# Kernel optimization log

Measured on AMD Instinct MI355X. Metric: run time of the kernel, lower is better.

Reference implementation:

```python
import jax, jax.numpy as jnp
import numpy as np

N, F = 8192, 1024


def _lin_params(key, out_f, in_f):
    kw, kb = jax.random.split(key)
    w = jax.random.normal(kw, (out_f, in_f), dtype=jnp.float32) * 0.02
    b = jax.random.normal(kb, (out_f,), dtype=jnp.float32) * 0.02
    return w, b


def setup_inputs() -> dict:
    key = jax.random.key(0)
    ks = jax.random.split(key, 11)
    X = jax.random.normal(ks[0], (N, F), dtype=jnp.float32)
    A = jax.random.uniform(ks[1], (N, N), dtype=jnp.float32)
    W1_w, W1_b = _lin_params(ks[2], 512, F)
    t1_w, t1_b = _lin_params(ks[3], 1, 512)
    r1_w, r1_b = _lin_params(ks[4], 1, 512)
    W2_w, W2_b = _lin_params(ks[5], 256, 512)
    t2_w, t2_b = _lin_params(ks[6], 1, 256)
    r2_w, r2_b = _lin_params(ks[7], 1, 256)
    W3_w, W3_b = _lin_params(ks[8], 64, 256)
    t3_w, t3_b = _lin_params(ks[9], 1, 64)
    r3_w, r3_b = _lin_params(ks[10], 1, 64)
    return dict(X=X, A=A,
                W1_w=W1_w, W1_b=W1_b, t1_w=t1_w, t1_b=t1_b, r1_w=r1_w, r1_b=r1_b,
                W2_w=W2_w, W2_b=W2_b, t2_w=t2_w, t2_b=t2_b, r2_w=r2_w, r2_b=r2_b,
                W3_w=W3_w, W3_b=W3_b, t3_w=t3_w, t3_b=t3_b, r3_w=r3_w, r3_b=r3_b)


def _gat_layer(H, A, W_w, W_b, t_w, t_b, r_w, r_b):
    Z = jax.nn.relu(H @ W_w.T + W_b)                     # [N, out]
    t = (Z @ t_w.T + t_b)[:, 0]                          # [N] = vkt(Z)
    r = (Z @ r_w.T + r_b)[:, 0]                          # [N] = vkr(Z)
    # M_s = A * vkt(Z).T  -> M_s[i,j] = A[i,j] * t[j]
    # M_r = (A * vkr(Z).T).T -> M_r[i,j] = A[j,i] * r[i]
    M = A * t[None, :] + A.T * r[:, None]
    att = jax.nn.softmax(jax.nn.sigmoid(M), axis=1)      # torch default dim=1 for 2D
    return att @ Z


def reference(X, A,
              W1_w, W1_b, t1_w, t1_b, r1_w, r1_b,
              W2_w, W2_b, t2_w, t2_b, r2_w, r2_b,
              W3_w, W3_b, t3_w, t3_b, r3_w, r3_b):
    H1 = _gat_layer(X, A, W1_w, W1_b, t1_w, t1_b, r1_w, r1_b)
    H2 = _gat_layer(H1, A, W2_w, W2_b, t2_w, t2_b, r2_w, r2_b)
    H3 = _gat_layer(H2, A, W3_w, W3_b, t3_w, t3_b, r3_w, r3_b)
    return H3
```

## Files before the change

kernel.cpp:

```cpp
#include <hip/hip_runtime.h>
#include <math.h>

#define NN 8192

typedef __attribute__((ext_vector_type(8))) short short8;
typedef __attribute__((ext_vector_type(4))) float f32x4;

__device__ __forceinline__ float bf2f(unsigned short u) {
    unsigned int x = ((unsigned int)u) << 16;
    return __builtin_bit_cast(float, x);
}
__device__ __forceinline__ unsigned int cvt_pk_bf16(float lo, float hi) {
    unsigned int r;
    asm("v_cvt_pk_bf16_f32 %0, %1, %2" : "=v"(r) : "v"(lo), "v"(hi));
    return r;
}
__device__ __forceinline__ float fast_sigexp(float x) {
    float s = __builtin_amdgcn_rcpf(1.0f + __expf(-x));
    return __expf(s);
}
__device__ __forceinline__ void gload16(const void* g, void* l) {
    __builtin_amdgcn_global_load_lds(
        (const __attribute__((address_space(1))) unsigned int*)g,
        (__attribute__((address_space(3))) unsigned int*)l, 16, 0, 0);
}

__global__ __launch_bounds__(256) void cvt_bf16(
    const float* __restrict__ src, unsigned short* __restrict__ dst)
{
    size_t idx = ((size_t)blockIdx.x * 256 + threadIdx.x) * 8;
    float4 a = *(const float4*)(src + idx);
    float4 b = *(const float4*)(src + idx + 4);
    uint4 o = { cvt_pk_bf16(a.x, a.y), cvt_pk_bf16(a.z, a.w),
                cvt_pk_bf16(b.x, b.y), cvt_pk_bf16(b.z, b.w) };
    *(uint4*)(dst + idx) = o;
}

template<typename AT> struct ARow;
template<> struct ARow<unsigned short> {
    struct Raw { uint4 a, b; };
    static __device__ __forceinline__ Raw ld(const unsigned short* p) {
        Raw r; r.a = ((const uint4*)p)[0]; r.b = ((const uint4*)p)[1]; return r;
    }
    static __device__ __forceinline__ void cvt(const Raw& r, float* d) {
        unsigned int wd[8] = {r.a.x, r.a.y, r.a.z, r.a.w, r.b.x, r.b.y, r.b.z, r.b.w};
        #pragma unroll
        for (int k = 0; k < 8; ++k) {
            d[2*k]   = __builtin_bit_cast(float, wd[k] << 16);
            d[2*k+1] = __builtin_bit_cast(float, wd[k] & 0xFFFF0000u);
        }
    }
};
template<> struct ARow<float> {
    struct Raw { float4 v[4]; };
    static __device__ __forceinline__ Raw ld(const float* p) {
        Raw r;
        r.v[0] = ((const float4*)p)[0]; r.v[1] = ((const float4*)p)[1];
        r.v[2] = ((const float4*)p)[2]; r.v[3] = ((const float4*)p)[3];
        return r;
    }
    static __device__ __forceinline__ void cvt(const Raw& r, float* d) {
        #pragma unroll
        for (int q = 0; q < 4; ++q) {
            d[4*q+0] = r.v[q].x; d[4*q+1] = r.v[q].y;
            d[4*q+2] = r.v[q].z; d[4*q+3] = r.v[q].w;
        }
    }
};
struct AcStageF32 {
    static __device__ __forceinline__ void st(const ARow<float>::Raw& rw, unsigned short* dst) {
        float v[16];
        ARow<float>::cvt(rw, v);
        unsigned int d[8];
        #pragma unroll
        for (int k = 0; k < 8; ++k) d[k] = cvt_pk_bf16(v[2*k], v[2*k+1]);
        uint4 s0 = {d[0], d[1], d[2], d[3]};
        uint4 s1 = {d[4], d[5], d[6], d[7]};
        ((uint4*)dst)[0] = s0;
        ((uint4*)dst)[1] = s1;
    }
};

__global__ __launch_bounds__(256) void proj_mfma(
    const unsigned short* __restrict__ Hbf,
    const unsigned short* __restrict__ Wbf,
    const float* __restrict__ bias,
    unsigned short* __restrict__ Zt,
    int K, int O)
{
    constexpr int MT = 4, NT = 2;
    __shared__ unsigned short smem[12288];
    const int tid = threadIdx.x;
    const int w = tid >> 6;
    const int lane = tid & 63;
    const int quad = lane >> 4;
    const int m16 = lane & 15;
    const int i0 = blockIdx.y * 128;
    const int o0 = blockIdx.x * 64;
    const int wm = w & 1;
    const int wn = w >> 1;

    const char* gpa[2]; unsigned int loa[2];
    #pragma unroll
    for (int n = 0; n < 2; ++n) {
        int o16 = n * 256 + w * 64 + lane;
        int row = o16 >> 2, ch = o16 & 3;
        int sc = ch ^ ((row >> 1) & 3);
        gpa[n] = (const char*)(Hbf + (size_t)(i0 + row) * K) + sc * 16;
        loa[n] = n * 4096 + w * 1024 + lane * 16;
    }
    const char* gpb; unsigned int lob_;
    {
        int o16 = w * 64 + lane;
        int row = o16 >> 2, ch = o16 & 3;
        int sc = ch ^ ((row >> 1) & 3);
        gpb = (const char*)(Wbf + (size_t)(o0 + row) * K) + sc * 16;
        lob_ = 8192 + w * 1024 + lane * 16;
    }
    int aoff[MT], boff[NT];
    #pragma unroll
    for (int mt = 0; mt < MT; ++mt) {
        int row = wm * 64 + mt * 16 + m16;
        int sc = quad ^ ((row >> 1) & 3);
        aoff[mt] = row * 32 + sc * 8;
    }
    #pragma unroll
    for (int nt = 0; nt < NT; ++nt) {
        int row = wn * 32 + nt * 16 + m16;
        int sc = quad ^ ((row >> 1) & 3);
        boff[nt] = 4096 + row * 32 + sc * 8;
    }
    f32x4 acc[MT][NT];
    #pragma unroll
    for (int mt = 0; mt < MT; ++mt)
        #pragma unroll
        for (int nt = 0; nt < NT; ++nt)
            acc[mt][nt] = (f32x4){0.f, 0.f, 0.f, 0.f};

    gload16(gpa[0], (char*)smem + loa[0]);
    gload16(gpa[1], (char*)smem + loa[1]);
    gload16(gpb,    (char*)smem + lob_);
    __syncthreads();

    const int nk = K >> 5;
    for (int kk = 0; kk < nk; ++kk) {
        const int s = kk & 1;
        if (kk + 1 < nk) {
            char* dst = (char*)smem + (s ^ 1) * 12288;
            gload16(gpa[0] + (size_t)(kk + 1) * 64, dst + loa[0]);
            gload16(gpa[1] + (size_t)(kk + 1) * 64, dst + loa[1]);
            gload16(gpb    + (size_t)(kk + 1) * 64, dst + lob_);
        }
        const unsigned short* buf = smem + s * 6144;
        short8 af[MT], bf_[NT];
        #pragma unroll
        for (int mt = 0; mt < MT; ++mt) af[mt] = *(const short8*)(buf + aoff[mt]);
        #pragma unroll
        for (int nt = 0; nt < NT; ++nt) bf_[nt] = *(const short8*)(buf + boff[nt]);
        #pragma unroll
        for (int mt = 0; mt < MT; ++mt)
            #pragma unroll
            for (int nt = 0; nt < NT; ++nt)
                acc[mt][nt] = __builtin_amdgcn_mfma_f32_16x16x32_bf16(
                    af[mt], bf_[nt], acc[mt][nt], 0, 0, 0);
        __syncthreads();
    }
    #pragma unroll
    for (int nt = 0; nt < NT; ++nt) {
        int ol = wn * 32 + nt * 16 + m16;
        float bv = bias[o0 + ol];
        #pragma unroll
        for (int mt = 0; mt < MT; ++mt) {
            int il = wm * 64 + mt * 16 + quad * 4;
            float f0 = fmaxf(acc[mt][nt][0] + bv, 0.f);
            float f1 = fmaxf(acc[mt][nt][1] + bv, 0.f);
            float f2 = fmaxf(acc[mt][nt][2] + bv, 0.f);
            float f3 = fmaxf(acc[mt][nt][3] + bv, 0.f);
            uint2 pk = { cvt_pk_bf16(f0, f1), cvt_pk_bf16(f2, f3) };
            *(uint2*)&smem[ol * 136 + il] = pk;
        }
    }
    __syncthreads();
    #pragma unroll
    for (int c = 0; c < 4; ++c) {
        int cc = c * 256 + tid;
        int ol = cc >> 4;
        int ic = (cc & 15) << 3;
        *(uint4*)(Zt + (size_t)(o0 + ol) * NN + i0 + ic) = *(const uint4*)&smem[ol * 136 + ic];
    }
}

__global__ __launch_bounds__(256) void tr_zt(
    const unsigned short* __restrict__ Zt,
    const float* __restrict__ tw, const float* __restrict__ tb,
    const float* __restrict__ rw, const float* __restrict__ rb,
    float* __restrict__ t, float* __restrict__ r)
{
    const int i  = blockIdx.x * 256 + threadIdx.x;
    const int c0 = blockIdx.y * 64;
    float at = 0.f, ar = 0.f;
    for (int c = c0; c < c0 + 64; ++c) {
        float z = bf2f(Zt[(size_t)c * NN + i]);
        at = fmaf(z, tw[c], at);
        ar = fmaf(z, rw[c], ar);
    }
    if (blockIdx.y == 0) { at += tb[0]; ar += rb[0]; }
    atomicAdd(t + i, at);
    atomicAdd(r + i, ar);
}

template<int BN, typename AT>
__global__ __launch_bounds__(256) void attn_fused(
    const AT* __restrict__ A,
    const unsigned short* __restrict__ Zt,
    const float* __restrict__ t, const float* __restrict__ r,
    float* __restrict__ Hacc, float* __restrict__ denom,
    int O, int kcount)
{
    constexpr bool BFA = (sizeof(AT) == 2);
    constexpr int BM = 128, BK = 32;
    constexpr int MT = 4;
    constexpr int NT = BN / 32;
    constexpr int NB = (BN * BK * 2) / 4096;
    constexpr int BNK = BN * BK;
    __shared__ unsigned short As[BM * BK];
    __shared__ unsigned short Bs[2][BNK];
    __shared__ unsigned short Ac[2][BK * BM];
    const int tid  = threadIdx.x;
    const int w    = tid >> 6;
    const int lane = tid & 63;
    const int quad = lane >> 4;
    const int m16  = lane & 15;
    const int i0 = blockIdx.y * BM;
    const int c0 = blockIdx.x * BN;
    const int wm = w & 1;
    const int wn = w >> 1;
    const int jbase = blockIdx.z * kcount * BK;

    const int ci = tid >> 1;
    const int jh = tid & 1;
    const float ri = r[i0 + ci];
    const int si = (ci >> 1) & 3;
    unsigned short* asw0 = As + ci * 32 + (((jh * 2)    ) ^ si) * 8;
    unsigned short* asw1 = As + ci * 32 + (((jh * 2) + 1) ^ si) * 8;
    const int acrd = jh * 16 * BM + (ci ^ (jh << 5));

    const char* gpb[NB]; unsigned int lob[NB];
    #pragma unroll
    for (int n = 0; n < NB; ++n) {
        int o16 = n * 256 + w * 64 + lane;
        int row = o16 >> 2, ch = o16 & 3;
        int sc = ch ^ ((row >> 1) & 3);
        gpb[n] = (const char*)Zt + ((size_t)(c0 + row) * NN + jbase) * 2 + sc * 16;
        lob[n] = n * 4096 + w * 1024 + lane * 16;
    }
    const char* gpac[2] = {nullptr, nullptr};
    unsigned int loac[2] = {0, 0};
    const float* astage = nullptr;
    int acw_off = 0;
    if constexpr (BFA) {
        #pragma unroll
        for (int n = 0; n < 2; ++n) {
            int o16 = n * 256 + tid;
            int row = o16 >> 4;
            int c16 = (o16 & 15) ^ ((row >> 4) << 2);
            gpac[n] = (const char*)(A + (size_t)(jbase + row) * NN + i0 + c16 * 8);
            loac[n] = (unsigned int)(o16 * 16);
        }
    } else {
        const int sj = tid >> 3;
        const int sm = tid & 7;
        astage = (const float*)A + (size_t)(jbase + sj) * NN + i0 + sm * 16;
        acw_off = sj * BM + (((sm * 2) ^ ((sj >> 4) << 2)) * 8);
    }

    int aoff[MT], boff[NT];
    #pragma unroll
    for (int mt = 0; mt < MT; ++mt) {
        int row = wm * 64 + mt * 16 + m16;
        int sc = quad ^ ((row >> 1) & 3);
        aoff[mt] = row * 32 + sc * 8;
    }
    #pragma unroll
    for (int nt = 0; nt < NT; ++nt) {
        int row = wn * (BN / 2) + nt * 16 + m16;
        int sc = quad ^ ((row >> 1) & 3);
        boff[nt] = row * 32 + sc * 8;
    }

    f32x4 acc[MT][NT];
    #pragma unroll
    for (int mt = 0; mt < MT; ++mt)
        #pragma unroll
        for (int nt = 0; nt < NT; ++nt)
            acc[mt][nt] = (f32x4){0.f, 0.f, 0.f, 0.f};

    const AT* arow = A + (size_t)(i0 + ci) * NN + jbase + jh * 16;
    const float* tptr = t + jbase + jh * 16;

    #pragma unroll
    for (int n = 0; n < NB; ++n)
        gload16(gpb[n], (char*)(Bs[0]) + lob[n]);
    if constexpr (BFA) {
        gload16(gpac[0], (char*)(Ac[0]) + loac[0]);
        gload16(gpac[1], (char*)(Ac[0]) + loac[1]);
    } else {
        ARow<float>::Raw a0 = ARow<float>::ld(astage);
        AcStageF32::st(a0, &Ac[0][0] + acw_off);
    }
    typename ARow<AT>::Raw avr = ARow<AT>::ld(arow);
    float4 tvr0 = ((const float4*)tptr)[0];
    float4 tvr1 = ((const float4*)tptr)[1];
    float4 tvr2 = ((const float4*)tptr)[2];
    float4 tvr3 = ((const float4*)tptr)[3];
    __syncthreads();

    ARow<float>::Raw acr;
    float rsum = 0.f;
    for (int kk = 0; kk < kcount; ++kk) {
        const int b = kk & 1;
        if (kk + 1 < kcount) {
            #pragma unroll
            for (int n = 0; n < NB; ++n)
                gload16(gpb[n] + (size_t)(kk + 1) * 64, (char*)(Bs[b ^ 1]) + lob[n]);
            if constexpr (BFA) {
                gload16(gpac[0] + (size_t)(kk + 1) * (BK * NN * 2), (char*)(Ac[b ^ 1]) + loac[0]);
                gload16(gpac[1] + (size_t)(kk + 1) * (BK * NN * 2), (char*)(Ac[b ^ 1]) + loac[1]);
            } else {
                acr = ARow<float>::ld(astage + (size_t)(kk + 1) * BK * NN);
            }
        }
        float av[16];
        ARow<AT>::cvt(avr, av);
        float tf[16] = {tvr0.x, tvr0.y, tvr0.z, tvr0.w,
                        tvr1.x, tvr1.y, tvr1.z, tvr1.w,
                        tvr2.x, tvr2.y, tvr2.z, tvr2.w,
                        tvr3.x, tvr3.y, tvr3.z, tvr3.w};
        const unsigned short* acb = &Ac[b][0] + acrd;
        unsigned int wd[8];
        #pragma unroll
        for (int q = 0; q < 8; ++q) {
            float j0 = bf2f(acb[(2 * q) * BM]);
            float j1 = bf2f(acb[(2 * q + 1) * BM]);
            float x0 = fmaf(av[2 * q],     tf[2 * q],     j0 * ri);
            float x1 = fmaf(av[2 * q + 1], tf[2 * q + 1], j1 * ri);
            float p0 = fast_sigexp(x0);
            float p1 = fast_sigexp(x1);
            rsum += p0; rsum += p1;
            wd[q] = cvt_pk_bf16(p0, p1);
        }
        {
            uint4 s0 = {wd[0], wd[1], wd[2], wd[3]};
            uint4 s1 = {wd[4], wd[5], wd[6], wd[7]};
            *(uint4*)asw0 = s0;
            *(uint4*)asw1 = s1;
        }
        __syncthreads();
        if (kk + 1 < kcount) {
            avr = ARow<AT>::ld(arow + (size_t)(kk + 1) * BK);
            const float* tp = tptr + (kk + 1) * BK;
            tvr0 = ((const float4*)tp)[0];
            tvr1 = ((const float4*)tp)[1];
            tvr2 = ((const float4*)tp)[2];
            tvr3 = ((const float4*)tp)[3];
            if constexpr (!BFA)
                AcStageF32::st(acr, &Ac[b ^ 1][0] + acw_off);
        }
        {
            const unsigned short* bsb = Bs[b];
            short8 af[MT], bf_[NT];
            #pragma unroll
            for (int mt = 0; mt < MT; ++mt) af[mt] = *(const short8*)(As + aoff[mt]);
            #pragma unroll
            for (int nt = 0; nt < NT; ++nt) bf_[nt] = *(const short8*)(bsb + boff[nt]);
            #pragma unroll
            for (int mt = 0; mt < MT; ++mt)
                #pragma unroll
                for (int nt = 0; nt < NT; ++nt)
                    acc[mt][nt] = __builtin_amdgcn_mfma_f32_16x16x32_bf16(
                        af[mt], bf_[nt], acc[mt][nt], 0, 0, 0);
        }
        __syncthreads();
    }

    rsum += __shfl_xor(rsum, 1);
    if (jh == 0 && blockIdx.x == 0)
        atomicAdd(denom + i0 + ci, rsum);

    const int colb = c0 + wn * (BN / 2) + m16;
    #pragma unroll
    for (int mt = 0; mt < MT; ++mt) {
        int rowb = i0 + wm * 64 + mt * 16 + quad * 4;
        #pragma unroll
        for (int rg = 0; rg < 4; ++rg) {
            float* orow = Hacc + (size_t)(rowb + rg) * O + colb;
            #pragma unroll
            for (int nt = 0; nt < NT; ++nt)
                atomicAdd(orow + nt * 16, acc[mt][nt][rg]);
        }
    }
}

__global__ __launch_bounds__(256) void norm_cvt(
    const float* __restrict__ Hacc, const float* __restrict__ denom,
    float* __restrict__ outf, unsigned short* __restrict__ outb, int O)
{
    const int gid = blockIdx.x * 256 + threadIdx.x;
    const int n4 = O >> 2;
    const int i = gid / n4;
    const int c = (gid % n4) << 2;
    float inv = __builtin_amdgcn_rcpf(denom[i]);
    float4 v = *(const float4*)(Hacc + (size_t)i * O + c);
    v.x *= inv; v.y *= inv; v.z *= inv; v.w *= inv;
    if (outf) {
        *(float4*)(outf + (size_t)i * O + c) = v;
    } else {
        uint2 o = { cvt_pk_bf16(v.x, v.y), cvt_pk_bf16(v.z, v.w) };
        *(uint2*)(outb + (size_t)i * O + c) = o;
    }
}

extern "C" void kernel_launch(void* const* d_in, const int* in_sizes, int n_in,
                              void* d_out, int out_size, void* d_ws, size_t ws_size,
                              hipStream_t stream)
{
    (void)in_sizes; (void)n_in; (void)out_size;
    const float* X = (const float*)d_in[0];
    const float* A = (const float*)d_in[1];
    const float* Wws[3] = {(const float*)d_in[2],  (const float*)d_in[8],  (const float*)d_in[14]};
    const float* Wbs[3] = {(const float*)d_in[3],  (const float*)d_in[9],  (const float*)d_in[15]};
    const float* tws[3] = {(const float*)d_in[4],  (const float*)d_in[10], (const float*)d_in[16]};
    const float* tbs[3] = {(const float*)d_in[5],  (const float*)d_in[11], (const float*)d_in[17]};
    const float* rws[3] = {(const float*)d_in[6],  (const float*)d_in[12], (const float*)d_in[18]};
    const float* rbs[3] = {(const float*)d_in[7],  (const float*)d_in[13], (const float*)d_in[19]};
    const int Ks[3] = {1024, 512, 256};
    const int Os[3] = {512, 256, 64};
    const int Zs[3] = {8, 16, 16};
    float* out = (float*)d_out;
    char* ws = (char*)d_ws;
    const size_t MB = (size_t)1 << 20;

    unsigned short* HbfX = (unsigned short*)(ws);
    unsigned short* Hbf2 = (unsigned short*)(ws + 16 * MB);
    unsigned short* Zt   = (unsigned short*)(ws + 24 * MB);
    float*          Hacc = (float*)(ws + 32 * MB);
    unsigned short* Wbf  = (unsigned short*)(ws + 48 * MB);
    float* tv = (float*)(ws + 50 * MB);
    float* rv = tv + NN;
    float* dv = rv + NN;
    unsigned short* Abf = (unsigned short*)(ws + 51 * MB);
    const bool useAbf = (ws_size >= 180 * MB);

    unsigned short* WbfL[3] = {Wbf, Wbf + 512 * 1024, Wbf + 512 * 1024 + 256 * 512};

    cvt_bf16<<<(NN * 1024) / 2048, 256, 0, stream>>>(X, HbfX);
    for (int L = 0; L < 3; ++L)
        cvt_bf16<<<(Os[L] * Ks[L]) / 2048, 256, 0, stream>>>(Wws[L], WbfL[L]);
    if (useAbf)
        cvt_bf16<<<(int)(((size_t)NN * NN) / 2048), 256, 0, stream>>>(A, Abf);

    const unsigned short* Hbf_in = HbfX;
    for (int L = 0; L < 3; ++L) {
        int K = Ks[L], O = Os[L];
        int zs = Zs[L];
        int kcount = NN / (zs * 32);
        proj_mfma<<<dim3(O / 64, NN / 128), 256, 0, stream>>>(
            Hbf_in, WbfL[L], Wbs[L], Zt, K, O);
        hipMemsetAsync(tv, 0, 96 * 1024, stream);
        tr_zt<<<dim3(NN / 256, O / 64), 256, 0, stream>>>(
            Zt, tws[L], tbs[L], rws[L], rbs[L], tv, rv);
        hipMemsetAsync(Hacc, 0, (size_t)NN * O * sizeof(float), stream);
        int gx = (O >= 256) ? O / 256 : 1;
        dim3 grid(gx, NN / 128, zs);
        if (useAbf) {
            if (O >= 256)
                attn_fused<256, unsigned short><<<grid, 256, 0, stream>>>(
                    Abf, Zt, tv, rv, Hacc, dv, O, kcount);
            else
                attn_fused<64, unsigned short><<<grid, 256, 0, stream>>>(
                    Abf, Zt, tv, rv, Hacc, dv, O, kcount);
        } else {
            if (O >= 256)
                attn_fused<256, float><<<grid, 256, 0, stream>>>(
                    A, Zt, tv, rv, Hacc, dv, O, kcount);
            else
                attn_fused<64, float><<<grid, 256, 0, stream>>>(
                    A, Zt, tv, rv, Hacc, dv, O, kcount);
        }
        float* outf = (L == 2) ? out : nullptr;
        unsigned short* outb = (L == 2) ? nullptr : Hbf2;
        norm_cvt<<<(NN / 256) * (O / 4), 256, 0, stream>>>(Hacc, dv, outf, outb, O);
        Hbf_in = Hbf2;
    }
}
```

Measured before the change: 920.3 us.

## Double-buffer attention tile, drop second barrier, deepen Ac prefetch, halve split-K

The attention kernel now double-buffers the As (probability) tile, which removes the trailing per-iteration barrier. It issues the B and A-transpose prefetches after the first barrier, with A-transpose staged two iterations ahead. MFMA blocks are wrapped in s_setprio to favour matrix issue, the row-sum is skipped in blocks that do not write the denominator, and the split-K factor Zs is halved, which reduces atomic accumulation traffic but also parallelism. The extra LDS buffer may lower occupancy, and the restructured barrier ordering carries race risk.

Result: faster. 849.1 us (-7.7%).

```diff
diff --git a/kernel.cpp b/kernel.cpp
--- a/kernel.cpp
+++ b/kernel.cpp
@@ -157,12 +157,14 @@
         for (int mt = 0; mt < MT; ++mt) af[mt] = *(const short8*)(buf + aoff[mt]);
         #pragma unroll
         for (int nt = 0; nt < NT; ++nt) bf_[nt] = *(const short8*)(buf + boff[nt]);
+        __builtin_amdgcn_s_setprio(1);
         #pragma unroll
         for (int mt = 0; mt < MT; ++mt)
             #pragma unroll
             for (int nt = 0; nt < NT; ++nt)
                 acc[mt][nt] = __builtin_amdgcn_mfma_f32_16x16x32_bf16(
                     af[mt], bf_[nt], acc[mt][nt], 0, 0, 0);
+        __builtin_amdgcn_s_setprio(0);
         __syncthreads();
     }
     #pragma unroll
@@ -223,7 +225,8 @@
     constexpr int NT = BN / 32;
     constexpr int NB = (BN * BK * 2) / 4096;
     constexpr int BNK = BN * BK;
-    __shared__ unsigned short As[BM * BK];
+    constexpr size_t ACB = (size_t)BK * NN * sizeof(AT);
+    __shared__ unsigned short As[2][BM * BK];
     __shared__ unsigned short Bs[2][BNK];
     __shared__ unsigned short Ac[2][BK * BM];
     const int tid  = threadIdx.x;
@@ -236,13 +239,14 @@
     const int wm = w & 1;
     const int wn = w >> 1;
     const int jbase = blockIdx.z * kcount * BK;
+    const bool x0 = (blockIdx.x == 0);
 
     const int ci = tid >> 1;
     const int jh = tid & 1;
     const float ri = r[i0 + ci];
     const int si = (ci >> 1) & 3;
-    unsigned short* asw0 = As + ci * 32 + (((jh * 2)    ) ^ si) * 8;
-    unsigned short* asw1 = As + ci * 32 + (((jh * 2) + 1) ^ si) * 8;
+    const int aswo0 = ci * 32 + (((jh * 2)    ) ^ si) * 8;
+    const int aswo1 = ci * 32 + (((jh * 2) + 1) ^ si) * 8;
     const int acrd = jh * 16 * BM + (ci ^ (jh << 5));
 
     const char* gpb[NB]; unsigned int lob[NB];
@@ -304,9 +308,14 @@
     if constexpr (BFA) {
         gload16(gpac[0], (char*)(Ac[0]) + loac[0]);
         gload16(gpac[1], (char*)(Ac[0]) + loac[1]);
+        if (kcount > 1) {
+            gload16(gpac[0] + ACB, (char*)(Ac[1]) + loac[0]);
+            gload16(gpac[1] + ACB, (char*)(Ac[1]) + loac[1]);
+        }
     } else {
-        ARow<float>::Raw a0 = ARow<float>::ld(astage);
-        AcStageF32::st(a0, &Ac[0][0] + acw_off);
+        AcStageF32::st(ARow<float>::ld(astage), &Ac[0][0] + acw_off);
+        if (kcount > 1)
+            AcStageF32::st(ARow<float>::ld(astage + (size_t)BK * NN), &Ac[1][0] + acw_off);
     }
     typename ARow<AT>::Raw avr = ARow<AT>::ld(arow);
     float4 tvr0 = ((const float4*)tptr)[0];
@@ -315,21 +324,9 @@
     float4 tvr3 = ((const float4*)tptr)[3];
     __syncthreads();
 
-    ARow<float>::Raw acr;
     float rsum = 0.f;
     for (int kk = 0; kk < kcount; ++kk) {
         const int b = kk & 1;
-        if (kk + 1 < kcount) {
-            #pragma unroll
-            for (int n = 0; n < NB; ++n)
-                gload16(gpb[n] + (size_t)(kk + 1) * 64, (char*)(Bs[b ^ 1]) + lob[n]);
-            if constexpr (BFA) {
-                gload16(gpac[0] + (size_t)(kk + 1) * (BK * NN * 2), (char*)(Ac[b ^ 1]) + loac[0]);
-                gload16(gpac[1] + (size_t)(kk + 1) * (BK * NN * 2), (char*)(Ac[b ^ 1]) + loac[1]);
-            } else {
-                acr = ARow<float>::ld(astage + (size_t)(kk + 1) * BK * NN);
-            }
-        }
         float av[16];
         ARow<AT>::cvt(avr, av);
         float tf[16] = {tvr0.x, tvr0.y, tvr0.z, tvr0.w,
@@ -342,20 +339,35 @@
         for (int q = 0; q < 8; ++q) {
             float j0 = bf2f(acb[(2 * q) * BM]);
             float j1 = bf2f(acb[(2 * q + 1) * BM]);
-            float x0 = fmaf(av[2 * q],     tf[2 * q],     j0 * ri);
-            float x1 = fmaf(av[2 * q + 1], tf[2 * q + 1], j1 * ri);
-            float p0 = fast_sigexp(x0);
-            float p1 = fast_sigexp(x1);
-            rsum += p0; rsum += p1;
+            float x0v = fmaf(av[2 * q],     tf[2 * q],     j0 * ri);
+            float x1v = fmaf(av[2 * q + 1], tf[2 * q + 1], j1 * ri);
+            float p0 = fast_sigexp(x0v);
+            float p1 = fast_sigexp(x1v);
+            if (x0) { rsum += p0; rsum += p1; }
             wd[q] = cvt_pk_bf16(p0, p1);
         }
         {
             uint4 s0 = {wd[0], wd[1], wd[2], wd[3]};
             uint4 s1 = {wd[4], wd[5], wd[6], wd[7]};
-            *(uint4*)asw0 = s0;
-            *(uint4*)asw1 = s1;
+            *(uint4*)(&As[b][0] + aswo0) = s0;
+            *(uint4*)(&As[b][0] + aswo1) = s1;
         }
         __syncthreads();
+        if (kk + 1 < kcount) {
+            #pragma unroll
+            for (int n = 0; n < NB; ++n)
+                gload16(gpb[n] + (size_t)(kk + 1) * 64, (char*)(Bs[b ^ 1]) + lob[n]);
+        }
+        if constexpr (BFA) {
+            if (kk + 2 < kcount) {
+                gload16(gpac[0] + (size_t)(kk + 2) * ACB, (char*)(Ac[b]) + loac[0]);
+                gload16(gpac[1] + (size_t)(kk + 2) * ACB, (char*)(Ac[b]) + loac[1]);
+            }
+        } else {
+            if (kk + 2 < kcount)
+                AcStageF32::st(ARow<float>::ld(astage + (size_t)(kk + 2) * BK * NN),
+                               &Ac[b][0] + acw_off);
+        }
         if (kk + 1 < kcount) {
             avr = ARow<AT>::ld(arow + (size_t)(kk + 1) * BK);
             const float* tp = tptr + (kk + 1) * BK;
@@ -363,28 +375,28 @@
             tvr1 = ((const float4*)tp)[1];
             tvr2 = ((const float4*)tp)[2];
             tvr3 = ((const float4*)tp)[3];
-            if constexpr (!BFA)
-                AcStageF32::st(acr, &Ac[b ^ 1][0] + acw_off);
         }
         {
+            const unsigned short* asb = &As[b][0];
             const unsigned short* bsb = Bs[b];
             short8 af[MT], bf_[NT];
             #pragma unroll
-            for (int mt = 0; mt < MT; ++mt) af[mt] = *(const short8*)(As + aoff[mt]);
+            for (int mt = 0; mt < MT; ++mt) af[mt] = *(const short8*)(asb + aoff[mt]);
             #pragma unroll
             for (int nt = 0; nt < NT; ++nt) bf_[nt] = *(const short8*)(bsb + boff[nt]);
+            __builtin_amdgcn_s_setprio(1);
             #pragma unroll
             for (int mt = 0; mt < MT; ++mt)
                 #pragma unroll
                 for (int nt = 0; nt < NT; ++nt)
                     acc[mt][nt] = __builtin_amdgcn_mfma_f32_16x16x32_bf16(
                         af[mt], bf_[nt], acc[mt][nt], 0, 0, 0);
-        }
-        __syncthreads();
+            __builtin_amdgcn_s_setprio(0);
+        }
     }
 
     rsum += __shfl_xor(rsum, 1);
-    if (jh == 0 && blockIdx.x == 0)
+    if (jh == 0 && x0)
         atomicAdd(denom + i0 + ci, rsum);
 
     const int colb = c0 + wn * (BN / 2) + m16;
@@ -435,7 +447,7 @@
     const float* rbs[3] = {(const float*)d_in[7],  (const float*)d_in[13], (const float*)d_in[19]};
     const int Ks[3] = {1024, 512, 256};
     const int Os[3] = {512, 256, 64};
-    const int Zs[3] = {8, 16, 16};
+    const int Zs[3] = {4, 8, 8};
     float* out = (float*)d_out;
     char* ws = (char*)d_ws;
     const size_t MB = (size_t)1 << 20;
```
